# Kernel optimization log

Hardware: AMD Instinct MI355X
Metric: run time of the kernel (lower is better)

Reference implementation:

```python
import jax, jax.numpy as jnp
import numpy as np

N = 100000      # n_nodes
D = 64          # in_features (= out_features)
H = 4           # attention heads
DK = D // H     # per-head dim
E = 1600000     # num edges (avg degree 16)
STEP = 0.25     # ODE euler step size
NSTEPS = 4      # integrate t in [0, 1]
ALPHA = 0.2     # LeakyReLU negative slope


def setup_inputs() -> dict:
    key = jax.random.key(0)
    k1, k2, k3, k4 = jax.random.split(key, 4)
    x = jax.random.normal(k1, (N, D), dtype=jnp.float32)
    edge_index = jax.random.randint(k2, (2, E), 0, N, dtype=jnp.int32)
    edge_weight = jax.random.uniform(k3, (E,), dtype=jnp.float32)
    # HamAgg.weight: init.eye_ -> identity [D, D]
    W = jnp.eye(D, dtype=jnp.float32)
    # HAM_GATConv.a: xavier_normal_ on shape (2*d_k, 1, 1), gain=1.414
    a = jax.random.normal(k4, (2 * DK,), dtype=jnp.float32) * (1.414 * np.sqrt(2.0 / (2 * DK + 1)))
    return {"x": x, "edge_index": edge_index, "edge_weight": edge_weight, "W": W, "a": a}


def reference(x, edge_index, edge_weight, W, a):
    # ---- Hamiltonian ODE block (args.vt == 'fc', odemap 'h1extend') ----
    # xt = hstack([x, x @ W.T]); euler-integrate canonical Hamiltonian flow
    # dq/dt = p, dp/dt = -q over t in [0,1] with step 0.25; keep first D dims.
    q = x
    p = x @ W.T
    for _ in range(NSTEPS):
        q, p = q + STEP * p, p - STEP * q
    xt = q  # out_x = out[..., :D]

    row, col = edge_index[0], edge_index[1]

    # ---- HAM_GATConv attention (W_x = x @ I = x) ----
    # h[n, head, k] = xt[n, head*DK + k]
    h = xt.reshape(N, H, DK)
    a_src, a_dst = a[:DK], a[DK:]
    s_src = h @ a_src   # [N, H] per-node source contribution
    s_dst = h @ a_dst   # [N, H] per-node dest contribution
    score = jax.nn.leaky_relu(s_src[row] + s_dst[col], ALPHA)  # [E, H]

    # segment softmax grouped by destination (edge[1])
    seg_max = jax.ops.segment_max(score, col, num_segments=N)  # [N, H]
    seg_max = jnp.where(jnp.isfinite(seg_max), seg_max, 0.0)
    e = jnp.exp(score - seg_max[col])
    denom = jax.ops.segment_sum(e, col, num_segments=N)
    att = e / (denom[col] + 1e-16)  # [E, H]

    # ---- mean over heads of per-head spmm == single spmm with mean attention ----
    # spmm: out[row[e]] += att[e] * xt[col[e]]
    w = att.mean(axis=1)  # [E]
    out = jax.ops.segment_sum(w[:, None] * xt[col], row, num_segments=N)  # [N, D]
    return out
```

## Files before the change

### kernel.cpp

```cpp
#include <hip/hip_runtime.h>
#include <hip/hip_bf16.h>


#define LRELU(v) ((v) > 0.0f ? (v) : 0.2f * (v))

#define EC 4096
#define BSC 256
#define BSR 128
#define DS 4
#define SLOTS 4

typedef __attribute__((ext_vector_type(8))) short bf16x8;
typedef __attribute__((ext_vector_type(4))) float f32x4;

__device__ __forceinline__ float bf16_to_f32(unsigned short u) {
    return __uint_as_float((unsigned int)u << 16);
}
__device__ __forceinline__ float bflo(unsigned int u) {
    return __uint_as_float(u << 16);
}
__device__ __forceinline__ float bfhi(unsigned int u) {
    return __uint_as_float(u & 0xFFFF0000u);
}
__device__ __forceinline__ unsigned short f32_to_bf16(float f) {
    __hip_bfloat16 h = __float2bfloat16(f);
    return *reinterpret_cast<unsigned short*>(&h);
}

__global__ __launch_bounds__(256) void k_geff(const float* __restrict__ W,
                                              const float* __restrict__ a,
                                              unsigned short* __restrict__ geff16,
                                              float c1, float c2) {
    int t = threadIdx.x;
    int k = t & 63, h = t >> 6;
    float ssrc = 0.0f, sdst = 0.0f;
#pragma unroll
    for (int d = 0; d < 16; ++d) {
        float w = W[(h * 16 + d) * 64 + k];
        ssrc += w * a[d];
        sdst += w * a[16 + d];
    }
    float gsrc = c2 * ssrc, gdst = c2 * sdst;
    if ((k >> 4) == h) {
        gsrc += c1 * a[k & 15];
        gdst += c1 * a[16 + (k & 15)];
    }
    unsigned short sh = f32_to_bf16(gsrc);
    unsigned short sl = f32_to_bf16(gsrc - bf16_to_f32(sh));
    unsigned short dh = f32_to_bf16(gdst);
    unsigned short dl = f32_to_bf16(gdst - bf16_to_f32(dh));
    geff16[h * 64 + k] = sh;
    geff16[(4 + h) * 64 + k] = dh;
    geff16[(8 + h) * 64 + k] = sl;
    geff16[(12 + h) * 64 + k] = dl;
}

__global__ __launch_bounds__(256) void k_node(const float* __restrict__ x,
                                              const float* __restrict__ W,
                                              const unsigned short* __restrict__ geff16,
                                              unsigned short* __restrict__ xt16,
                                              float* __restrict__ s_src,
                                              float* __restrict__ s_dst,
                                              int n, float c1, float c2) {
    int wave = threadIdx.x >> 6;
    int lane = threadIdx.x & 63;
    int nb = blockIdx.x * 64 + wave * 16;
    if (nb >= n) return;
    int colg = lane & 15;
    int grp = lane >> 4;
    int k0 = grp << 3;

    bf16x8 wf[4][2];
#pragma unroll
    for (int ct = 0; ct < 4; ++ct) {
#pragma unroll
        for (int ks = 0; ks < 2; ++ks) {
            const float* wr = W + (size_t)(ct * 16 + colg) * 64 + k0 + ks * 32;
            float4 w0 = *(const float4*)(wr);
            float4 w1 = *(const float4*)(wr + 4);
            bf16x8 f;
            f[0] = (short)f32_to_bf16(w0.x); f[1] = (short)f32_to_bf16(w0.y);
            f[2] = (short)f32_to_bf16(w0.z); f[3] = (short)f32_to_bf16(w0.w);
            f[4] = (short)f32_to_bf16(w1.x); f[5] = (short)f32_to_bf16(w1.y);
            f[6] = (short)f32_to_bf16(w1.z); f[7] = (short)f32_to_bf16(w1.w);
            wf[ct][ks] = f;
        }
    }
    bf16x8 gf[2];
#pragma unroll
    for (int ks = 0; ks < 2; ++ks)
        gf[ks] = *(const bf16x8*)(geff16 + colg * 64 + k0 + ks * 32);

    int arow = nb + colg;
    if (arow >= n) arow = n - 1;
    const float* xr = x + (size_t)arow * 64 + k0;
    bf16x8 af[2];
#pragma unroll
    for (int ks = 0; ks < 2; ++ks) {
        float4 x0 = *(const float4*)(xr + ks * 32);
        float4 x1 = *(const float4*)(xr + ks * 32 + 4);
        bf16x8 f;
        f[0] = (short)f32_to_bf16(x0.x); f[1] = (short)f32_to_bf16(x0.y);
        f[2] = (short)f32_to_bf16(x0.z); f[3] = (short)f32_to_bf16(x0.w);
        f[4] = (short)f32_to_bf16(x1.x); f[5] = (short)f32_to_bf16(x1.y);
        f[6] = (short)f32_to_bf16(x1.z); f[7] = (short)f32_to_bf16(x1.w);
        af[ks] = f;
    }

    f32x4 acc[5];
#pragma unroll
    for (int i = 0; i < 5; ++i) acc[i] = (f32x4){0.f, 0.f, 0.f, 0.f};
#pragma unroll
    for (int ct = 0; ct < 4; ++ct) {
        acc[ct] = __builtin_amdgcn_mfma_f32_16x16x32_bf16(af[0], wf[ct][0], acc[ct], 0, 0, 0);
        acc[ct] = __builtin_amdgcn_mfma_f32_16x16x32_bf16(af[1], wf[ct][1], acc[ct], 0, 0, 0);
    }
    acc[4] = __builtin_amdgcn_mfma_f32_16x16x32_bf16(af[0], gf[0], acc[4], 0, 0, 0);
    acc[4] = __builtin_amdgcn_mfma_f32_16x16x32_bf16(af[1], gf[1], acc[4], 0, 0, 0);

#pragma unroll
    for (int ct = 0; ct < 4; ++ct) {
        int col = ct * 16 + colg;
#pragma unroll
        for (int rr = 0; rr < 4; ++rr) {
            int node = nb + grp * 4 + rr;
            if (node < n) {
                float xv = x[(size_t)node * 64 + col];
                float xtv = c1 * xv + c2 * acc[ct][rr];
                xt16[(size_t)node * 64 + col] = f32_to_bf16(xtv);
            }
        }
    }
#pragma unroll
    for (int rr = 0; rr < 4; ++rr) {
        float v = acc[4][rr];
        float tot = v + __shfl_xor(v, 8, 64);
        int node = nb + grp * 4 + rr;
        if (node < n) {
            if (colg < 4) s_src[node * 4 + colg] = tot;
            else if (colg < 8) s_dst[node * 4 + (colg - 4)] = tot;
        }
    }
}

__global__ __launch_bounds__(256) void k_hist(const int* __restrict__ row,
                                              const int* __restrict__ col,
                                              int* __restrict__ Hr,
                                              int* __restrict__ Hc,
                                              int e, int nblk, int nbr, int nbc) {
    __shared__ int hr[1024];
    __shared__ int hc[512];
    int t = threadIdx.x;
    for (int i = t; i < 1024; i += 256) hr[i] = 0;
    for (int i = t; i < 512; i += 256) hc[i] = 0;
    __syncthreads();
    int base = blockIdx.x * EC;
#pragma unroll
    for (int j = 0; j < EC / 256; ++j) {
        int i = base + t + j * 256;
        if (i < e) {
            atomicAdd(&hr[row[i] >> 7], 1);
            atomicAdd(&hc[col[i] >> 8], 1);
        }
    }
    __syncthreads();
    for (int b = t; b < nbr; b += 256) Hr[(size_t)b * nblk + blockIdx.x] = hr[b];
    for (int b = t; b < nbc; b += 256) Hc[(size_t)b * nblk + blockIdx.x] = hc[b];
}

__global__ __launch_bounds__(256) void k_scanH2(int* __restrict__ Hr,
                                                int* __restrict__ Hc,
                                                int* __restrict__ BtotR,
                                                int* __restrict__ BtotC,
                                                int nblk, int nbr) {
    __shared__ int vals[512];
    __shared__ int part[256];
    int t = threadIdx.x;
    int bb = blockIdx.x;
    int* Hb;
    int* Btot;
    if (bb < nbr) {
        Hb = Hr + (size_t)bb * nblk;
        Btot = BtotR + bb;
    } else {
        Hb = Hc + (size_t)(bb - nbr) * nblk;
        Btot = BtotC + (bb - nbr);
    }
    for (int i = t; i < nblk; i += 256) vals[i] = Hb[i];
    __syncthreads();
    int c0 = t * 2;
    int s = 0;
#pragma unroll
    for (int j = 0; j < 2; ++j)
        if (c0 + j < nblk) s += vals[c0 + j];
    part[t] = s;
    __syncthreads();
    for (int d = 1; d < 256; d <<= 1) {
        int add = (t >= d) ? part[t - d] : 0;
        __syncthreads();
        part[t] += add;
        __syncthreads();
    }
    int run = part[t] - s;
#pragma unroll
    for (int j = 0; j < 2; ++j) {
        int i = c0 + j;
        if (i < nblk) {
            int v = vals[i];
            Hb[i] = run;
            run += v;
        }
    }
    if (t == 255) *Btot = part[255];
}

__global__ __launch_bounds__(256) void k_base2(const int* __restrict__ BtotR,
                                               int* __restrict__ BbR, int nbr,
                                               const int* __restrict__ BtotC,
                                               int* __restrict__ BbC, int nbc) {
    const int* Btot = (blockIdx.x == 0) ? BtotR : BtotC;
    int* Bbase = (blockIdx.x == 0) ? BbR : BbC;
    int nb = (blockIdx.x == 0) ? nbr : nbc;
    __shared__ int part[256];
    __shared__ int carry;
    int t = threadIdx.x;
    if (t == 0) carry = 0;
    __syncthreads();
    for (int base = 0; base < nb; base += 256) {
        int i = base + t;
        int v = (i < nb) ? Btot[i] : 0;
        part[t] = v;
        __syncthreads();
        for (int d = 1; d < 256; d <<= 1) {
            int add = (t >= d) ? part[t - d] : 0;
            __syncthreads();
            part[t] += add;
            __syncthreads();
        }
        if (i < nb) Bbase[i] = carry + part[t] - v;
        __syncthreads();
        if (t == 0) carry += part[255];
        __syncthreads();
    }
    if (t == 0) Bbase[nb] = carry;
}

__global__ __launch_bounds__(256) void k_scatter_dual(
    const int* __restrict__ row, const int* __restrict__ col,
    const int* __restrict__ Hr, const int* __restrict__ Hc,
    const int* __restrict__ BbR, const int* __restrict__ BbC,
    int* __restrict__ ebr, int* __restrict__ ebc,
    int e, int nblk, int nbr, int nbc) {
    __shared__ int curr[1024];
    __shared__ int curc[512];
    int t = threadIdx.x;
    int blk = blockIdx.x;
    for (int b = t; b < nbr; b += 256) curr[b] = BbR[b] + Hr[(size_t)b * nblk + blk];
    for (int b = t; b < nbc; b += 256) curc[b] = BbC[b] + Hc[(size_t)b * nblk + blk];
    __syncthreads();
    int base = blk * EC;
#pragma unroll
    for (int j = 0; j < EC / 256; ++j) {
        int i = base + t + j * 256;
        if (i < e) {
            int r = row[i], c = col[i];
            int pr = atomicAdd(&curr[r >> 7], 1);
            ebr[pr] = (c << 7) | (r & 127);
            int pc = atomicAdd(&curc[c >> 8], 1);
            ebc[pc] = (r << 8) | (c & 255);
        }
    }
}

__global__ __launch_bounds__(256) void k_denom_p(const int* __restrict__ ebc,
                                                 const int* __restrict__ BbC,
                                                 const float* __restrict__ s_src,
                                                 const float* __restrict__ s_dst,
                                                 float* __restrict__ part,
                                                 int n, int n4) {
    __shared__ float acc[BSC * 4];
    __shared__ float sd[BSC * 4];
    int t = threadIdx.x;
    int bucket = blockIdx.x >> 2;
    int slice = blockIdx.x & 3;
    int cbase = bucket << 8;
    for (int i = t; i < BSC * 4; i += 256) {
        acc[i] = 0.0f;
        int c4 = cbase * 4 + i;
        sd[i] = (c4 < n4) ? s_dst[c4] : 0.0f;
    }
    __syncthreads();
    int start = BbC[bucket], end = BbC[bucket + 1];
    int len = end - start;
    int i0 = start + (int)(((long long)len * slice) >> 2);
    int i1 = start + (int)(((long long)len * (slice + 1)) >> 2);
    for (int i = i0 + t; i < i1; i += 256) {
        int p = ebc[i];
        int r = p >> 8, cl = p & 255;
        float4 ss = *(const float4*)(s_src + (size_t)r * 4);
        atomicAdd(&acc[cl * 4 + 0], __expf(LRELU(ss.x + sd[cl * 4 + 0])));
        atomicAdd(&acc[cl * 4 + 1], __expf(LRELU(ss.y + sd[cl * 4 + 1])));
        atomicAdd(&acc[cl * 4 + 2], __expf(LRELU(ss.z + sd[cl * 4 + 2])));
        atomicAdd(&acc[cl * 4 + 3], __expf(LRELU(ss.w + sd[cl * 4 + 3])));
    }
    __syncthreads();
    float* ps = part + (size_t)slice * n4;
    for (int i = t; i < BSC * 4; i += 256) {
        int c4 = cbase * 4 + i;
        if (c4 < n4) ps[c4] = acc[i];
    }
}

__global__ __launch_bounds__(256) void k_comb(const float* __restrict__ part,
                                              const float* __restrict__ s_dst,
                                              float* __restrict__ sdr, int n4) {
    int idx = blockIdx.x * 256 + threadIdx.x;
    if (idx >= n4) return;
    float s = part[idx] + part[(size_t)n4 + idx] + part[(size_t)2 * n4 + idx] +
              part[(size_t)3 * n4 + idx];
    int c = idx >> 2, h = idx & 3;
    sdr[(size_t)c * 8 + h] = s_dst[idx];
    sdr[(size_t)c * 8 + 4 + h] = 1.0f / (s + 1e-16f);
}

__global__ __launch_bounds__(256) void k_sort2(const int* __restrict__ ebr,
                                               const int* __restrict__ BbR,
                                               const float* __restrict__ s_src,
                                               const float* __restrict__ sdr,
                                               int* __restrict__ rowptr,
                                               int2* __restrict__ cwp,
                                               int n, int e) {
    __shared__ int cnt[BSR];
    __shared__ int pfx[BSR];
    __shared__ int cur[BSR];
    __shared__ float ssh[BSR * 4];
    int t = threadIdx.x;
    int b = blockIdx.x;
    int rbase = b << 7;
    if (t < BSR) cnt[t] = 0;
    for (int i = t; i < BSR * 4; i += 256) {
        int g = rbase * 4 + i;
        ssh[i] = (g < n * 4) ? s_src[g] : 0.0f;
    }
    __syncthreads();
    int start = BbR[b], end = BbR[b + 1];
    for (int i = start + t; i < end; i += 256)
        atomicAdd(&cnt[ebr[i] & 127], 1);
    __syncthreads();
    if (t < BSR) pfx[t] = cnt[t];
    __syncthreads();
    for (int d = 1; d < BSR; d <<= 1) {
        int v = (t < BSR && t >= d) ? pfx[t - d] : 0;
        __syncthreads();
        if (t < BSR) pfx[t] += v;
        __syncthreads();
    }
    if (t < BSR) {
        int excl = start + pfx[t] - cnt[t];
        cur[t] = excl;
        int r = rbase + t;
        if (r < n) rowptr[r] = excl;
    }
    if (b == 0 && t == 0) rowptr[n] = e;
    __syncthreads();
    for (int i = start + t; i < end; i += 256) {
        int p = ebr[i];
        int rl = p & 127, c = p >> 7;
        float4 sd = *(const float4*)(sdr + (size_t)c * 8);
        float4 rd = *(const float4*)(sdr + (size_t)c * 8 + 4);
        float wv = __expf(LRELU(ssh[rl * 4 + 0] + sd.x)) * rd.x +
                   __expf(LRELU(ssh[rl * 4 + 1] + sd.y)) * rd.y +
                   __expf(LRELU(ssh[rl * 4 + 2] + sd.z)) * rd.z +
                   __expf(LRELU(ssh[rl * 4 + 3] + sd.w)) * rd.w;
        int pos = atomicAdd(&cur[rl], 1);
        cwp[pos] = make_int2(c << 6, __float_as_int(0.25f * wv));
    }
}

__global__ __launch_bounds__(256) void k_aggr(const int* __restrict__ rowptr,
                                              const int2* __restrict__ cwp,
                                              const unsigned short* __restrict__ xt16,
                                              float* __restrict__ out, int n, int e) {
    int r = blockIdx.x * 4 + (threadIdx.x >> 6);
    if (r >= n) return;
    int lane = threadIdx.x & 63;
    int g = lane >> 3;
    unsigned le = (lane & 7) << 3;
    int start = rowptr[r], end = rowptr[r + 1];
    float acc[8];
#pragma unroll
    for (int j = 0; j < 8; ++j) acc[j] = 0.0f;
    for (int base = start; base < end; base += SLOTS * 8) {
        int m = end - base;
        if (m > SLOTS * 8) m = SLOTS * 8;
        int nk = (m + 7) >> 3;
        uint4 u[SLOTS];
        float wv[SLOTS];
#pragma unroll
        for (int k = 0; k < SLOTS; ++k) {
            if (k < nk) {
                int idx = base + k * 8 + g;
                int idc = idx < e ? idx : e - 1;
                int2 cw = cwp[idc];
                wv[k] = (idx < end) ? __int_as_float(cw.y) : 0.0f;
                u[k] = *(const uint4*)(xt16 + ((unsigned)cw.x + le));
            }
        }
#pragma unroll
        for (int k = 0; k < SLOTS; ++k) {
            if (k < nk) {
                acc[0] = fmaf(wv[k], bflo(u[k].x), acc[0]);
                acc[1] = fmaf(wv[k], bfhi(u[k].x), acc[1]);
                acc[2] = fmaf(wv[k], bflo(u[k].y), acc[2]);
                acc[3] = fmaf(wv[k], bfhi(u[k].y), acc[3]);
                acc[4] = fmaf(wv[k], bflo(u[k].z), acc[4]);
                acc[5] = fmaf(wv[k], bfhi(u[k].z), acc[5]);
                acc[6] = fmaf(wv[k], bflo(u[k].w), acc[6]);
                acc[7] = fmaf(wv[k], bfhi(u[k].w), acc[7]);
            }
        }
    }
#pragma unroll
    for (int off = 8; off <= 32; off <<= 1) {
#pragma unroll
        for (int j = 0; j < 8; ++j) acc[j] += __shfl_xor(acc[j], off, 64);
    }
    if (lane < 8) {
        float4 a0 = {acc[0], acc[1], acc[2], acc[3]};
        float4 a1 = {acc[4], acc[5], acc[6], acc[7]};
        *(float4*)(out + (size_t)r * 64 + le) = a0;
        *(float4*)(out + (size_t)r * 64 + le + 4) = a1;
    }
}

extern "C" void kernel_launch(void* const* d_in, const int* in_sizes, int n_in,
                              void* d_out, int out_size, void* d_ws, size_t ws_size,
                              hipStream_t stream) {
    const float* x = (const float*)d_in[0];
    const int* ei = (const int*)d_in[1];
    const float* W = (const float*)d_in[3];
    const float* a = (const float*)d_in[4];
    int n = in_sizes[0] / 64;
    int e = in_sizes[1] / 2;
    const int* row = ei;
    const int* col = ei + e;
    float* out = (float*)d_out;

    int nblk = (e + EC - 1) / EC;
    int nbr = (n + BSR - 1) / BSR;
    int nbc = (n + BSC - 1) / BSC;
    int n4 = n * 4;

    size_t o = 0;
    auto take = [&](size_t cnt) {
        size_t p = o;
        o += (cnt + 3) & ~(size_t)3;
        return p;
    };
    int* wsi = (int*)d_ws;
    unsigned short* xt16 = (unsigned short*)(wsi + take((size_t)n * 32));
    float* s_src = (float*)(wsi + take((size_t)n * 4));
    float* s_dst = (float*)(wsi + take((size_t)n * 4));
    float* sdr = (float*)(wsi + take((size_t)n * 8));
    float* part = (float*)(wsi + take((size_t)n * 4 * DS));
    unsigned short* geff16 = (unsigned short*)(wsi + take(512));
    int* Hr = wsi + take((size_t)nbr * nblk);
    int* Hc = wsi + take((size_t)nbc * nblk);
    int* BtotR = wsi + take(nbr);
    int* BbR = wsi + take(nbr + 1);
    int* BtotC = wsi + take(nbc);
    int* BbC = wsi + take(nbc + 1);
    int* ebr = wsi + take(e);
    int* cwbuf = wsi + take((size_t)2 * e);
    int* ebc = cwbuf;
    int2* cwp = (int2*)cwbuf;
    int* rowptr = wsi + take(n + 1);

    float aq = 1.f, bq = 0.f, ap = 0.f, bp = 1.f;
    for (int i = 0; i < 4; ++i) {
        float naq = aq + 0.25f * ap, nbq = bq + 0.25f * bp;
        float nap = ap - 0.25f * aq, nbp = bp - 0.25f * bq;
        aq = naq; bq = nbq; ap = nap; bp = nbp;
    }

    k_geff<<<1, 256, 0, stream>>>(W, a, geff16, aq, bq);
    k_node<<<(n + 63) / 64, 256, 0, stream>>>(x, W, geff16, xt16, s_src, s_dst,
                                              n, aq, bq);
    k_hist<<<nblk, 256, 0, stream>>>(row, col, Hr, Hc, e, nblk, nbr, nbc);
    k_scanH2<<<nbr + nbc, 256, 0, stream>>>(Hr, Hc, BtotR, BtotC, nblk, nbr);
    k_base2<<<2, 256, 0, stream>>>(BtotR, BbR, nbr, BtotC, BbC, nbc);
    k_scatter_dual<<<nblk, 256, 0, stream>>>(row, col, Hr, Hc, BbR, BbC,
                                             ebr, ebc, e, nblk, nbr, nbc);
    k_denom_p<<<nbc * DS, 256, 0, stream>>>(ebc, BbC, s_src, s_dst, part, n, n4);
    k_comb<<<(n4 + 255) / 256, 256, 0, stream>>>(part, s_dst, sdr, n4);
    k_sort2<<<nbr, 256, 0, stream>>>(ebr, BbR, s_src, sdr, rowptr, cwp, n, e);
    k_aggr<<<(n + 3) / 4, 256, 0, stream>>>(rowptr, cwp, xt16, out, n, e);
}
```

Before: 288.8 us.

## Merge node/geff/histogram kernels and fold base scan into scatter

Combines k_geff, k_node and k_hist into one launch, k_front. Node blocks compute the effective attention vectors into shared memory, and the remaining blocks build the edge histograms. The block-total prefix scan (k_base2) is folded into k_scatter_dual, so every scatter block recomputes the small scan redundantly and block 0 writes BbR/BbC. This cuts three kernel launches and the serialization between them, and lets the node and histogram work run concurrently. In exchange, every node block recomputes geff, and every scatter block does extra scan work and barriers.

```diff
diff --git a/kernel.cpp b/kernel.cpp
--- a/kernel.cpp
+++ b/kernel.cpp
@@ -27,145 +27,146 @@
     return *reinterpret_cast<unsigned short*>(&h);
 }
 
-__global__ __launch_bounds__(256) void k_geff(const float* __restrict__ W,
-                                              const float* __restrict__ a,
-                                              unsigned short* __restrict__ geff16,
-                                              float c1, float c2) {
-    int t = threadIdx.x;
-    int k = t & 63, h = t >> 6;
-    float ssrc = 0.0f, sdst = 0.0f;
-#pragma unroll
-    for (int d = 0; d < 16; ++d) {
-        float w = W[(h * 16 + d) * 64 + k];
-        ssrc += w * a[d];
-        sdst += w * a[16 + d];
-    }
-    float gsrc = c2 * ssrc, gdst = c2 * sdst;
-    if ((k >> 4) == h) {
-        gsrc += c1 * a[k & 15];
-        gdst += c1 * a[16 + (k & 15)];
-    }
-    unsigned short sh = f32_to_bf16(gsrc);
-    unsigned short sl = f32_to_bf16(gsrc - bf16_to_f32(sh));
-    unsigned short dh = f32_to_bf16(gdst);
-    unsigned short dl = f32_to_bf16(gdst - bf16_to_f32(dh));
-    geff16[h * 64 + k] = sh;
-    geff16[(4 + h) * 64 + k] = dh;
-    geff16[(8 + h) * 64 + k] = sl;
-    geff16[(12 + h) * 64 + k] = dl;
-}
-
-__global__ __launch_bounds__(256) void k_node(const float* __restrict__ x,
-                                              const float* __restrict__ W,
-                                              const unsigned short* __restrict__ geff16,
-                                              unsigned short* __restrict__ xt16,
-                                              float* __restrict__ s_src,
-                                              float* __restrict__ s_dst,
-                                              int n, float c1, float c2) {
-    int wave = threadIdx.x >> 6;
-    int lane = threadIdx.x & 63;
-    int nb = blockIdx.x * 64 + wave * 16;
-    if (nb >= n) return;
-    int colg = lane & 15;
-    int grp = lane >> 4;
-    int k0 = grp << 3;
-
-    bf16x8 wf[4][2];
-#pragma unroll
-    for (int ct = 0; ct < 4; ++ct) {
-#pragma unroll
-        for (int ks = 0; ks < 2; ++ks) {
-            const float* wr = W + (size_t)(ct * 16 + colg) * 64 + k0 + ks * 32;
-            float4 w0 = *(const float4*)(wr);
-            float4 w1 = *(const float4*)(wr + 4);
-            bf16x8 f;
-            f[0] = (short)f32_to_bf16(w0.x); f[1] = (short)f32_to_bf16(w0.y);
-            f[2] = (short)f32_to_bf16(w0.z); f[3] = (short)f32_to_bf16(w0.w);
-            f[4] = (short)f32_to_bf16(w1.x); f[5] = (short)f32_to_bf16(w1.y);
-            f[6] = (short)f32_to_bf16(w1.z); f[7] = (short)f32_to_bf16(w1.w);
-            wf[ct][ks] = f;
-        }
-    }
-    bf16x8 gf[2];
-#pragma unroll
-    for (int ks = 0; ks < 2; ++ks)
-        gf[ks] = *(const bf16x8*)(geff16 + colg * 64 + k0 + ks * 32);
-
-    int arow = nb + colg;
-    if (arow >= n) arow = n - 1;
-    const float* xr = x + (size_t)arow * 64 + k0;
-    bf16x8 af[2];
-#pragma unroll
-    for (int ks = 0; ks < 2; ++ks) {
-        float4 x0 = *(const float4*)(xr + ks * 32);
-        float4 x1 = *(const float4*)(xr + ks * 32 + 4);
-        bf16x8 f;
-        f[0] = (short)f32_to_bf16(x0.x); f[1] = (short)f32_to_bf16(x0.y);
-        f[2] = (short)f32_to_bf16(x0.z); f[3] = (short)f32_to_bf16(x0.w);
-        f[4] = (short)f32_to_bf16(x1.x); f[5] = (short)f32_to_bf16(x1.y);
-        f[6] = (short)f32_to_bf16(x1.z); f[7] = (short)f32_to_bf16(x1.w);
-        af[ks] = f;
-    }
-
-    f32x4 acc[5];
-#pragma unroll
-    for (int i = 0; i < 5; ++i) acc[i] = (f32x4){0.f, 0.f, 0.f, 0.f};
-#pragma unroll
-    for (int ct = 0; ct < 4; ++ct) {
-        acc[ct] = __builtin_amdgcn_mfma_f32_16x16x32_bf16(af[0], wf[ct][0], acc[ct], 0, 0, 0);
-        acc[ct] = __builtin_amdgcn_mfma_f32_16x16x32_bf16(af[1], wf[ct][1], acc[ct], 0, 0, 0);
-    }
-    acc[4] = __builtin_amdgcn_mfma_f32_16x16x32_bf16(af[0], gf[0], acc[4], 0, 0, 0);
-    acc[4] = __builtin_amdgcn_mfma_f32_16x16x32_bf16(af[1], gf[1], acc[4], 0, 0, 0);
-
-#pragma unroll
-    for (int ct = 0; ct < 4; ++ct) {
-        int col = ct * 16 + colg;
-#pragma unroll
-        for (int rr = 0; rr < 4; ++rr) {
-            int node = nb + grp * 4 + rr;
-            if (node < n) {
-                float xv = x[(size_t)node * 64 + col];
-                float xtv = c1 * xv + c2 * acc[ct][rr];
-                xt16[(size_t)node * 64 + col] = f32_to_bf16(xtv);
-            }
-        }
-    }
-#pragma unroll
-    for (int rr = 0; rr < 4; ++rr) {
-        float v = acc[4][rr];
-        float tot = v + __shfl_xor(v, 8, 64);
-        int node = nb + grp * 4 + rr;
-        if (node < n) {
-            if (colg < 4) s_src[node * 4 + colg] = tot;
-            else if (colg < 8) s_dst[node * 4 + (colg - 4)] = tot;
-        }
-    }
-}
-
-__global__ __launch_bounds__(256) void k_hist(const int* __restrict__ row,
-                                              const int* __restrict__ col,
-                                              int* __restrict__ Hr,
-                                              int* __restrict__ Hc,
-                                              int e, int nblk, int nbr, int nbc) {
+__global__ __launch_bounds__(256) void k_front(const float* __restrict__ x,
+                                               const float* __restrict__ W,
+                                               const float* __restrict__ a,
+                                               const int* __restrict__ row,
+                                               const int* __restrict__ col,
+                                               unsigned short* __restrict__ xt16,
+                                               float* __restrict__ s_src,
+                                               float* __restrict__ s_dst,
+                                               int* __restrict__ Hr,
+                                               int* __restrict__ Hc,
+                                               int n, int e, int nbn, int nblk,
+                                               int nbr, int nbc,
+                                               float c1, float c2) {
+    __shared__ unsigned short geffL[16 * 64];
     __shared__ int hr[1024];
     __shared__ int hc[512];
     int t = threadIdx.x;
-    for (int i = t; i < 1024; i += 256) hr[i] = 0;
-    for (int i = t; i < 512; i += 256) hc[i] = 0;
-    __syncthreads();
-    int base = blockIdx.x * EC;
-#pragma unroll
-    for (int j = 0; j < EC / 256; ++j) {
-        int i = base + t + j * 256;
-        if (i < e) {
-            atomicAdd(&hr[row[i] >> 7], 1);
-            atomicAdd(&hc[col[i] >> 8], 1);
-        }
-    }
-    __syncthreads();
-    for (int b = t; b < nbr; b += 256) Hr[(size_t)b * nblk + blockIdx.x] = hr[b];
-    for (int b = t; b < nbc; b += 256) Hc[(size_t)b * nblk + blockIdx.x] = hc[b];
+    if (blockIdx.x < nbn) {
+        {
+            int k = t & 63, h = t >> 6;
+            float ssrc = 0.0f, sdst = 0.0f;
+#pragma unroll
+            for (int d = 0; d < 16; ++d) {
+                float w = W[(h * 16 + d) * 64 + k];
+                ssrc += w * a[d];
+                sdst += w * a[16 + d];
+            }
+            float gsrc = c2 * ssrc, gdst = c2 * sdst;
+            if ((k >> 4) == h) {
+                gsrc += c1 * a[k & 15];
+                gdst += c1 * a[16 + (k & 15)];
+            }
+            unsigned short sh = f32_to_bf16(gsrc);
+            unsigned short sl = f32_to_bf16(gsrc - bf16_to_f32(sh));
+            unsigned short dh = f32_to_bf16(gdst);
+            unsigned short dl = f32_to_bf16(gdst - bf16_to_f32(dh));
+            geffL[h * 64 + k] = sh;
+            geffL[(4 + h) * 64 + k] = dh;
+            geffL[(8 + h) * 64 + k] = sl;
+            geffL[(12 + h) * 64 + k] = dl;
+        }
+        __syncthreads();
+
+        int wave = t >> 6;
+        int lane = t & 63;
+        int nb = blockIdx.x * 64 + wave * 16;
+        if (nb >= n) return;
+        int colg = lane & 15;
+        int grp = lane >> 4;
+        int k0 = grp << 3;
+
+        bf16x8 wf[4][2];
+#pragma unroll
+        for (int ct = 0; ct < 4; ++ct) {
+#pragma unroll
+            for (int ks = 0; ks < 2; ++ks) {
+                const float* wr = W + (size_t)(ct * 16 + colg) * 64 + k0 + ks * 32;
+                float4 w0 = *(const float4*)(wr);
+                float4 w1 = *(const float4*)(wr + 4);
+                bf16x8 f;
+                f[0] = (short)f32_to_bf16(w0.x); f[1] = (short)f32_to_bf16(w0.y);
+                f[2] = (short)f32_to_bf16(w0.z); f[3] = (short)f32_to_bf16(w0.w);
+                f[4] = (short)f32_to_bf16(w1.x); f[5] = (short)f32_to_bf16(w1.y);
+                f[6] = (short)f32_to_bf16(w1.z); f[7] = (short)f32_to_bf16(w1.w);
+                wf[ct][ks] = f;
+            }
+        }
+        bf16x8 gf[2];
+#pragma unroll
+        for (int ks = 0; ks < 2; ++ks)
+            gf[ks] = *(const bf16x8*)(geffL + colg * 64 + k0 + ks * 32);
+
+        int arow = nb + colg;
+        if (arow >= n) arow = n - 1;
+        const float* xr = x + (size_t)arow * 64 + k0;
+        bf16x8 af[2];
+#pragma unroll
+        for (int ks = 0; ks < 2; ++ks) {
+            float4 x0 = *(const float4*)(xr + ks * 32);
+            float4 x1 = *(const float4*)(xr + ks * 32 + 4);
+            bf16x8 f;
+            f[0] = (short)f32_to_bf16(x0.x); f[1] = (short)f32_to_bf16(x0.y);
+            f[2] = (short)f32_to_bf16(x0.z); f[3] = (short)f32_to_bf16(x0.w);
+            f[4] = (short)f32_to_bf16(x1.x); f[5] = (short)f32_to_bf16(x1.y);
+            f[6] = (short)f32_to_bf16(x1.z); f[7] = (short)f32_to_bf16(x1.w);
+            af[ks] = f;
+        }
+
+        f32x4 acc[5];
+#pragma unroll
+        for (int i = 0; i < 5; ++i) acc[i] = (f32x4){0.f, 0.f, 0.f, 0.f};
+#pragma unroll
+        for (int ct = 0; ct < 4; ++ct) {
+            acc[ct] = __builtin_amdgcn_mfma_f32_16x16x32_bf16(af[0], wf[ct][0], acc[ct], 0, 0, 0);
+            acc[ct] = __builtin_amdgcn_mfma_f32_16x16x32_bf16(af[1], wf[ct][1], acc[ct], 0, 0, 0);
+        }
+        acc[4] = __builtin_amdgcn_mfma_f32_16x16x32_bf16(af[0], gf[0], acc[4], 0, 0, 0);
+        acc[4] = __builtin_amdgcn_mfma_f32_16x16x32_bf16(af[1], gf[1], acc[4], 0, 0, 0);
+
+#pragma unroll
+        for (int ct = 0; ct < 4; ++ct) {
+            int c = ct * 16 + colg;
+#pragma unroll
+            for (int rr = 0; rr < 4; ++rr) {
+                int node = nb + grp * 4 + rr;
+                if (node < n) {
+                    float xv = x[(size_t)node * 64 + c];
+                    float xtv = c1 * xv + c2 * acc[ct][rr];
+                    xt16[(size_t)node * 64 + c] = f32_to_bf16(xtv);
+                }
+            }
+        }
+#pragma unroll
+        for (int rr = 0; rr < 4; ++rr) {
+            float v = acc[4][rr];
+            float tot = v + __shfl_xor(v, 8, 64);
+            int node = nb + grp * 4 + rr;
+            if (node < n) {
+                if (colg < 4) s_src[node * 4 + colg] = tot;
+                else if (colg < 8) s_dst[node * 4 + (colg - 4)] = tot;
+            }
+        }
+    } else {
+        int blk = blockIdx.x - nbn;
+        for (int i = t; i < 1024; i += 256) hr[i] = 0;
+        for (int i = t; i < 512; i += 256) hc[i] = 0;
+        __syncthreads();
+        int base = blk * EC;
+#pragma unroll
+        for (int j = 0; j < EC / 256; ++j) {
+            int i = base + t + j * 256;
+            if (i < e) {
+                atomicAdd(&hr[row[i] >> 7], 1);
+                atomicAdd(&hc[col[i] >> 8], 1);
+            }
+        }
+        __syncthreads();
+        for (int b = t; b < nbr; b += 256) Hr[(size_t)b * nblk + blk] = hr[b];
+        for (int b = t; b < nbc; b += 256) Hc[(size_t)b * nblk + blk] = hc[b];
+    }
 }
 
 __global__ __launch_bounds__(256) void k_scanH2(int* __restrict__ Hr,
@@ -214,22 +215,27 @@
     if (t == 255) *Btot = part[255];
 }
 
-__global__ __launch_bounds__(256) void k_base2(const int* __restrict__ BtotR,
-                                               int* __restrict__ BbR, int nbr,
-                                               const int* __restrict__ BtotC,
-                                               int* __restrict__ BbC, int nbc) {
-    const int* Btot = (blockIdx.x == 0) ? BtotR : BtotC;
-    int* Bbase = (blockIdx.x == 0) ? BbR : BbC;
-    int nb = (blockIdx.x == 0) ? nbr : nbc;
+__global__ __launch_bounds__(256) void k_scatter_dual(
+    const int* __restrict__ row, const int* __restrict__ col,
+    const int* __restrict__ Hr, const int* __restrict__ Hc,
+    const int* __restrict__ BtotR, const int* __restrict__ BtotC,
+    int* __restrict__ BbR, int* __restrict__ BbC,
+    int* __restrict__ ebr, int* __restrict__ ebc,
+    int e, int nblk, int nbr, int nbc) {
+    __shared__ int vals[1024];
     __shared__ int part[256];
-    __shared__ int carry;
+    __shared__ int curr[1024];
+    __shared__ int curc[512];
     int t = threadIdx.x;
-    if (t == 0) carry = 0;
-    __syncthreads();
-    for (int base = 0; base < nb; base += 256) {
-        int i = base + t;
-        int v = (i < nb) ? Btot[i] : 0;
-        part[t] = v;
+    int blk = blockIdx.x;
+    for (int i = t; i < nbr; i += 256) vals[i] = BtotR[i];
+    __syncthreads();
+    {
+        int c0 = t * 4, s = 0;
+#pragma unroll
+        for (int j = 0; j < 4; ++j)
+            if (c0 + j < nbr) s += vals[c0 + j];
+        part[t] = s;
         __syncthreads();
         for (int d = 1; d < 256; d <<= 1) {
             int add = (t >= d) ? part[t - d] : 0;
@@ -237,26 +243,48 @@
             part[t] += add;
             __syncthreads();
         }
-        if (i < nb) Bbase[i] = carry + part[t] - v;
-        __syncthreads();
-        if (t == 0) carry += part[255];
-        __syncthreads();
-    }
-    if (t == 0) Bbase[nb] = carry;
-}
-
-__global__ __launch_bounds__(256) void k_scatter_dual(
-    const int* __restrict__ row, const int* __restrict__ col,
-    const int* __restrict__ Hr, const int* __restrict__ Hc,
-    const int* __restrict__ BbR, const int* __restrict__ BbC,
-    int* __restrict__ ebr, int* __restrict__ ebc,
-    int e, int nblk, int nbr, int nbc) {
-    __shared__ int curr[1024];
-    __shared__ int curc[512];
-    int t = threadIdx.x;
-    int blk = blockIdx.x;
-    for (int b = t; b < nbr; b += 256) curr[b] = BbR[b] + Hr[(size_t)b * nblk + blk];
-    for (int b = t; b < nbc; b += 256) curc[b] = BbC[b] + Hc[(size_t)b * nblk + blk];
+        int run = part[t] - s;
+#pragma unroll
+        for (int j = 0; j < 4; ++j) {
+            int i = c0 + j;
+            if (i < nbr) {
+                int v = vals[i];
+                curr[i] = run + Hr[(size_t)i * nblk + blk];
+                if (blk == 0) BbR[i] = run;
+                run += v;
+            }
+        }
+        if (blk == 0 && t == 255) BbR[nbr] = part[255];
+    }
+    __syncthreads();
+    for (int i = t; i < nbc; i += 256) vals[i] = BtotC[i];
+    __syncthreads();
+    {
+        int c0 = t * 4, s = 0;
+#pragma unroll
+        for (int j = 0; j < 4; ++j)
+            if (c0 + j < nbc) s += vals[c0 + j];
+        part[t] = s;
+        __syncthreads();
+        for (int d = 1; d < 256; d <<= 1) {
+            int add = (t >= d) ? part[t - d] : 0;
+            __syncthreads();
+            part[t] += add;
+            __syncthreads();
+        }
+        int run = part[t] - s;
+#pragma unroll
+        for (int j = 0; j < 4; ++j) {
+            int i = c0 + j;
+            if (i < nbc) {
+                int v = vals[i];
+                curc[i] = run + Hc[(size_t)i * nblk + blk];
+                if (blk == 0) BbC[i] = run;
+                run += v;
+            }
+        }
+        if (blk == 0 && t == 255) BbC[nbc] = part[255];
+    }
     __syncthreads();
     int base = blk * EC;
 #pragma unroll
@@ -449,6 +477,7 @@
     int nblk = (e + EC - 1) / EC;
     int nbr = (n + BSR - 1) / BSR;
     int nbc = (n + BSC - 1) / BSC;
+    int nbn = (n + 63) / 64;
     int n4 = n * 4;
 
     size_t o = 0;
@@ -463,7 +492,6 @@
     float* s_dst = (float*)(wsi + take((size_t)n * 4));
     float* sdr = (float*)(wsi + take((size_t)n * 8));
     float* part = (float*)(wsi + take((size_t)n * 4 * DS));
-    unsigned short* geff16 = (unsigned short*)(wsi + take(512));
     int* Hr = wsi + take((size_t)nbr * nblk);
     int* Hc = wsi + take((size_t)nbc * nblk);
     int* BtotR = wsi + take(nbr);
@@ -483,14 +511,13 @@
         aq = naq; bq = nbq; ap = nap; bp = nbp;
     }
 
-    k_geff<<<1, 256, 0, stream>>>(W, a, geff16, aq, bq);
-    k_node<<<(n + 63) / 64, 256, 0, stream>>>(x, W, geff16, xt16, s_src, s_dst,
-                                              n, aq, bq);
-    k_hist<<<nblk, 256, 0, stream>>>(row, col, Hr, Hc, e, nblk, nbr, nbc);
+    k_front<<<nbn + nblk, 256, 0, stream>>>(x, W, a, row, col, xt16, s_src,
+                                            s_dst, Hr, Hc, n, e, nbn, nblk,
+                                            nbr, nbc, aq, bq);
     k_scanH2<<<nbr + nbc, 256, 0, stream>>>(Hr, Hc, BtotR, BtotC, nblk, nbr);
-    k_base2<<<2, 256, 0, stream>>>(BtotR, BbR, nbr, BtotC, BbC, nbc);
-    k_scatter_dual<<<nblk, 256, 0, stream>>>(row, col, Hr, Hc, BbR, BbC,
-                                             ebr, ebc, e, nblk, nbr, nbc);
+    k_scatter_dual<<<nblk, 256, 0, stream>>>(row, col, Hr, Hc, BtotR, BtotC,
+                                             BbR, BbC, ebr, ebc, e, nblk,
+                                             nbr, nbc);
     k_denom_p<<<nbc * DS, 256, 0, stream>>>(ebc, BbC, s_src, s_dst, part, n, n4);
     k_comb<<<(n4 + 255) / 256, 256, 0, stream>>>(part, s_dst, sdr, n4);
     k_sort2<<<nbr, 256, 0, stream>>>(ebr, BbR, s_src, sdr, rowptr, cwp, n, e);
```

New measurement: 281.3 us. 1.03x faster.
